# Kernel optimization log

Hardware: AMD Instinct MI355X
Metric: run time of the kernel (lower is better)

Reference implementation:

```python
import jax, jax.numpy as jnp
from jax import lax
import numpy as np

B, IMG_H, IMG_W = 8, 256, 512
NUM_CLASSES, P = 20, 32
SCALE, TOPK, IOU_THR = 32.0, 100, 0.5


def conv2d(x, w, b, stride=1, pad=1):
    y = lax.conv_general_dilated(x, w, (stride, stride), [(pad, pad), (pad, pad)],
                                 dimension_numbers=('NCHW', 'OIHW', 'NCHW'))
    return y + b[None, :, None, None]


def bilinear_resize(img, out_h, out_w):
    # img: [..., H, W]; torch F.interpolate(mode='bilinear', align_corners=False)
    H, W = img.shape[-2], img.shape[-1]
    def idx_w(n_in, n_out):
        src = (jnp.arange(n_out, dtype=jnp.float32) + 0.5) * (n_in / n_out) - 0.5
        src = jnp.clip(src, 0.0, n_in - 1)
        i0 = jnp.floor(src).astype(jnp.int32)
        i1 = jnp.minimum(i0 + 1, n_in - 1)
        return i0, i1, src - i0.astype(jnp.float32)
    y0, y1, wy = idx_w(H, out_h)
    x0, x1, wx = idx_w(W, out_w)
    top = img[..., y0, :] * (1.0 - wy)[:, None] + img[..., y1, :] * wy[:, None]
    return top[..., x0] * (1.0 - wx) + top[..., x1] * wx


def generate_anchors(fh, fw):
    ys = (jnp.arange(fh, dtype=jnp.float32) + 0.5) * (IMG_H / fh)
    xs = (jnp.arange(fw, dtype=jnp.float32) + 0.5) * (IMG_W / fw)
    cy, cx = jnp.meshgrid(ys, xs, indexing='ij')
    h = SCALE / 2
    return jnp.stack([cx - h, cy - h, cx + h, cy + h], -1).reshape(-1, 4)


def delta_to_boxes(anchors, deltas):
    a_c = (anchors[:, :2] + anchors[:, 2:]) / 2
    a_wh = anchors[:, 2:] - anchors[:, :2]
    pc = a_c + deltas[..., :2] * a_wh
    pwh = a_wh * jnp.exp(deltas[..., 2:])
    return jnp.concatenate([pc - pwh / 2, pc + pwh / 2], -1)


def nms_single(boxes, scores, labels):
    # torchvision batched_nms: offset boxes per label, greedy NMS, return kept idxs
    N = boxes.shape[0]
    off = labels.astype(boxes.dtype) * (jnp.max(boxes) + 1.0)
    b = boxes + off[:, None]
    order = jnp.argsort(-scores)
    bs = b[order]
    area = (bs[:, 2] - bs[:, 0]) * (bs[:, 3] - bs[:, 1])
    lt = jnp.maximum(bs[:, None, :2], bs[None, :, :2])
    rb = jnp.minimum(bs[:, None, 2:], bs[None, :, 2:])
    wh = jnp.clip(rb - lt, 0.0)
    inter = wh[..., 0] * wh[..., 1]
    iou = inter / (area[:, None] + area[None, :] - inter + 1e-9)
    idxs = jnp.arange(N)
    def body(i, suppressed):
        keep_i = jnp.logical_not(suppressed[i])
        row = (iou[i] > IOU_THR) & (idxs > i)
        return jnp.where(keep_i, suppressed | row, suppressed)
    suppressed = lax.fori_loop(0, N, body, jnp.zeros(N, bool))
    keep_mask = ~suppressed
    rank = jnp.cumsum(keep_mask) - 1
    slots = jnp.where(keep_mask & (rank < TOPK), rank, TOPK)
    out = jnp.full(TOPK + 1, -1, jnp.int32).at[slots].set(order.astype(jnp.int32))
    return out[:TOPK]


def setup_inputs():
    key = jax.random.key(0)
    ks = jax.random.split(key, 17)
    def cw(k, o, i, kh, kw_):
        return jax.random.normal(k, (o, i, kh, kw_), jnp.float32) / np.sqrt(i * kh * kw_)
    return {
        'images': jax.random.normal(ks[0], (B, 3, IMG_H, IMG_W), jnp.float32),
        'w1': cw(ks[1], 64, 3, 3, 3),   'b1': jnp.zeros(64, jnp.float32),
        'w2': cw(ks[2], 128, 64, 3, 3), 'b2': jnp.zeros(128, jnp.float32),
        'w3': cw(ks[3], 256, 128, 3, 3),'b3': jnp.zeros(256, jnp.float32),
        'pw1': cw(ks[4], 256, 256, 3, 3), 'pb1': jnp.zeros(256, jnp.float32),
        'pw2': cw(ks[5], P, 256, 1, 1),   'pb2': jnp.zeros(P, jnp.float32),
        'cw_': cw(ks[6], NUM_CLASSES + 1, 256, 3, 3), 'cb': jnp.zeros(NUM_CLASSES + 1, jnp.float32),
        'bw': cw(ks[7], 4, 256, 3, 3),  'bb': jnp.zeros(4, jnp.float32),
        'kw': cw(ks[8], P, 256, 3, 3),  'kb': jnp.zeros(P, jnp.float32),
    }


def reference(images, w1, b1, w2, b2, w3, b3, pw1, pb1, pw2, pb2, cw_, cb, bw, bb, kw, kb):
    x = jax.nn.relu(conv2d(images, w1, b1, stride=2))
    x = jax.nn.relu(conv2d(x, w2, b2, stride=2))
    feat = jax.nn.relu(conv2d(x, w3, b3, stride=2))          # [B,256,32,64]
    proto = conv2d(jax.nn.relu(conv2d(feat, pw1, pb1)), pw2, pb2, pad=0)  # [B,P,32,64]
    fh, fw = feat.shape[2], feat.shape[3]
    def head(w, b, c):
        return conv2d(feat, w, b).transpose(0, 2, 3, 1).reshape(B, -1, c)
    cls = head(cw_, cb, NUM_CLASSES + 1)     # [B,N,C+1]
    box = head(bw, bb, 4)                    # [B,N,4]
    coef = head(kw, kb, P)                   # [B,N,P]
    anchors = generate_anchors(fh, fw)       # [N,4]
    probs = jax.nn.softmax(cls, -1)[..., :-1]
    scores = probs.max(-1)
    labels = probs.argmax(-1).astype(jnp.int32)
    boxes = delta_to_boxes(anchors, box)     # [B,N,4]
    keep = jax.vmap(nms_single)(boxes, scores, labels)   # [B,100], -1 pad
    valid = keep >= 0
    ki = jnp.clip(keep, 0)
    take = lambda a: jnp.take_along_axis(a, ki[..., None] if a.ndim == 3 else ki, axis=1)
    boxes_k = take(boxes) * valid[..., None]
    scores_k = take(scores) * valid
    labels_k = jnp.where(valid, take(labels), 0)
    coef_k = jnp.take_along_axis(coef, ki[..., None], axis=1)   # [B,100,P]
    m = jax.nn.sigmoid(jnp.einsum('bkp,bphw->bkhw', coef_k, proto))
    masks = bilinear_resize(m, IMG_H, IMG_W) > 0.5
    masks = masks & valid[..., None, None]
    return boxes_k, scores_k, labels_k, masks, valid
```

## Files before the change

kernel.cpp:

```cpp
#include <hip/hip_runtime.h>
#include <hip/hip_bf16.h>
#include <math.h>

#define BB 8
#define NCLS 21
#define NANCH 2048
#define TOPK_N 100

static const size_t OFF_X1HI = 0;
static const size_t OFF_X1LO = 34344960;
static const size_t OFF_X2HI = 68689920;
static const size_t OFF_X2LO = 86261760;
static const size_t OFF_FTHI = 103833600;
static const size_t OFF_FTLO = 113025024;
static const size_t OFF_WT1  = 122216448;
static const size_t OFF_A2H  = 122223616;
static const size_t OFF_A2L  = 122371072;
static const size_t OFF_A3H  = 122518528;
static const size_t OFF_A3L  = 123108352;
static const size_t OFF_AHH  = 123698176;
static const size_t OFF_AHL  = 123993088;
static const size_t OFF_AP1H = 124288000;
static const size_t OFF_AP1L = 125467648;
static const size_t OFF_WTP2 = 126647296;
static const size_t OFF_BH   = 126680064;
static const size_t OFF_HOUT = 126680576;
static const size_t OFF_P1   = 130874880;
static const size_t OFF_PROTO= 147652096;
static const size_t OFF_BOXES= 149749248;
static const size_t OFF_SCORES=150011392;
static const size_t OFF_LABELS=150076928;
static const size_t OFF_ORDER= 150142464;
static const size_t OFF_SB   = 150208000;
static const size_t OFF_IOU  = 150470144;
static const size_t OFF_KEEP = 154664448;
static const size_t OFF_MAXB = 154668032;
static const size_t OFF_M    = 154668544;

static const size_t OUT_BOXES  = 0;
static const size_t OUT_SCORES = 3200;
static const size_t OUT_LABELS = 4000;
static const size_t OUT_MASKS  = 4800;
static const size_t OUT_VALID  = 104862400;

typedef __attribute__((ext_vector_type(8))) short bf16x8;
typedef __attribute__((ext_vector_type(4))) float f32x4;

__device__ __forceinline__ unsigned encf(float f){
  unsigned u = __float_as_uint(f);
  return (u & 0x80000000u) ? ~u : (u | 0x80000000u);
}
__device__ __forceinline__ float decf(unsigned u){
  unsigned b = (u & 0x80000000u) ? (u & 0x7fffffffu) : ~u;
  return __uint_as_float(b);
}
__device__ __forceinline__ short f2bf(float f){
  __hip_bfloat16 h = __float2bfloat16(f);
  return *(short*)&h;
}
__device__ __forceinline__ float bf2f(short h){
  return __uint_as_float(((unsigned)(unsigned short)h) << 16);
}

template<int CH8,int Hp,int Wp>
__global__ void halok(short* __restrict__ hi, short* __restrict__ lo,
                      unsigned* __restrict__ maxb){
  constexpr int PER = 2*Wp + 2*(Hp-2);
  int i = blockIdx.x*256 + threadIdx.x;
  if (maxb && i < BB) maxb[i] = 0u;
  if (i >= BB*CH8*PER) return;
  int cell = i % PER; int bg = i / PER;
  int y, x;
  if (cell < Wp)        { y = 0;      x = cell; }
  else if (cell < 2*Wp) { y = Hp-1;   x = cell - Wp; }
  else { int r = cell - 2*Wp; y = 1 + (r>>1); x = (r&1) ? (Wp-1) : 0; }
  size_t ad = (((size_t)bg*Hp + y)*Wp + x)*8;
  bf16x8 z = (bf16x8){0,0,0,0,0,0,0,0};
  *(bf16x8*)(hi + ad) = z;
  *(bf16x8*)(lo + ad) = z;
}

template<int CIN,int COUT,int KK>
__global__ void packw(const float* __restrict__ w, float* __restrict__ wT){
  int i = blockIdx.x*256 + threadIdx.x;
  if (i >= CIN*KK*COUT) return;
  int co = i % COUT; int r = i / COUT;
  int ci = r / KK,  k = r % KK;
  wT[i] = w[(co*CIN + ci)*KK + k];
}

template<int CIN,int COUT>
__global__ void packA(const float* __restrict__ w, short* __restrict__ Ahi,
                      short* __restrict__ Alo){
  constexpr int K = CIN*9;
  constexpr int KS = K/32;
  int i = blockIdx.x*256 + threadIdx.x;
  if (i >= COUT*K) return;
  int sub  = i & 7;
  int lane = (i >> 3) & 63;
  int rest = i >> 9;
  int ks = rest % KS;
  int mt = rest / KS;
  int m = mt*16 + (lane & 15);
  int k = ks*32 + (lane >> 4)*8 + sub;
  int tap = k / CIN, ci = k - tap*CIN;
  float v = w[(m*CIN + ci)*9 + tap];
  short h = f2bf(v);
  Ahi[i] = h;
  Alo[i] = f2bf(v - bf2f(h));
}

__global__ void packAh(const float* __restrict__ cw, const float* __restrict__ bw,
                       const float* __restrict__ kw, const float* __restrict__ cb,
                       const float* __restrict__ bb, const float* __restrict__ kb,
                       short* __restrict__ Ahi, short* __restrict__ Alo,
                       float* __restrict__ bh){
  int i = blockIdx.x*256 + threadIdx.x;
  if (i < 64){
    float v = 0.f;
    if (i < 21) v = cb[i]; else if (i < 25) v = bb[i-21]; else if (i < 57) v = kb[i-25];
    bh[i] = v;
  }
  if (i >= 64*2304) return;
  constexpr int KS = 72;
  int sub  = i & 7;
  int lane = (i >> 3) & 63;
  int rest = i >> 9;
  int ks = rest % KS;
  int mt = rest / KS;
  int m = mt*16 + (lane & 15);
  int k = ks*32 + (lane >> 4)*8 + sub;
  int tap = k >> 8, ci = k & 255;
  float v = 0.f;
  if (m < 21)      v = cw[(m*256 + ci)*9 + tap];
  else if (m < 25) v = bw[((m-21)*256 + ci)*9 + tap];
  else if (m < 57) v = kw[((m-25)*256 + ci)*9 + tap];
  short h = f2bf(v);
  Ahi[i] = h;
  Alo[i] = f2bf(v - bf2f(h));
}

__global__ __launch_bounds__(256) void conv1k(const float* __restrict__ img,
    const float* __restrict__ wT, const float* __restrict__ bias,
    short* __restrict__ x1hi, short* __restrict__ x1lo){
  const int b   = blockIdx.z;
  const int co0 = blockIdx.y * 16;
  const int g   = blockIdx.x*256 + threadIdx.x;
  const int y  = g >> 7;
  const int x0 = (g & 127) << 1;

  float acc[16][2];
#pragma unroll
  for (int c=0;c<16;c++){
    float bv = bias[co0+c];
    acc[c][0] = bv; acc[c][1] = bv;
  }
  int   off[3][5];
  float msk[3][5];
#pragma unroll
  for (int kh=0;kh<3;kh++){
    int iy = y*2 - 1 + kh;
    bool okr = (iy >= 0) && (iy < 256);
    int ro = okr ? iy*512 : 0;
#pragma unroll
    for (int t=0;t<5;t++){
      int col = x0*2 - 1 + t;
      bool ok = okr && (col >= 0) && (col < 512);
      off[kh][t] = ok ? (ro + col) : 0;
      msk[kh][t] = ok ? 1.f : 0.f;
    }
  }
  const float* inb = img + (size_t)b*3*256*512;
  for (int ci=0; ci<3; ci++){
    const float* inc = inb + (size_t)ci*256*512;
    float v[3][5];
#pragma unroll
    for (int kh=0;kh<3;kh++)
#pragma unroll
      for (int t=0;t<5;t++)
        v[kh][t] = inc[off[kh][t]] * msk[kh][t];
    const float* wp = wT + ci*9*64 + co0;
#pragma unroll
    for (int kh=0;kh<3;kh++)
#pragma unroll
    for (int kw=0;kw<3;kw++){
      const float* wq = wp + (kh*3+kw)*64;
#pragma unroll
      for (int c=0;c<16;c++){
        float wv = wq[c];
        acc[c][0] = fmaf(wv, v[kh][2*0+kw], acc[c][0]);
        acc[c][1] = fmaf(wv, v[kh][2*1+kw], acc[c][1]);
      }
    }
  }
#pragma unroll
  for (int s=0;s<2;s++){
    short hv[16] __attribute__((aligned(16)));
    short lv[16] __attribute__((aligned(16)));
#pragma unroll
    for (int c=0;c<16;c++){
      float r = fmaxf(acc[c][s], 0.f);
      short h = f2bf(r);
      hv[c] = h;
      lv[c] = f2bf(r - bf2f(h));
    }
#pragma unroll
    for (int g2=0; g2<2; g2++){
      size_t ad = (((size_t)(b*8 + (co0>>3) + g2)*130 + (y+1))*258 + (x0+s+1))*8;
      *(bf16x8*)(x1hi + ad) = *(bf16x8*)(hv + g2*8);
      *(bf16x8*)(x1lo + ad) = *(bf16x8*)(lv + g2*8);
    }
  }
}

template<int CIN,int K,int M,int MW,int NW,int S,int IPH,int IPW,int NXB,
         bool SPLIT,bool STAGELO,int EMODE,int OPH,int OPW>
__global__ __launch_bounds__(NW*64) void cgemm_row(
    const short* __restrict__ Ahi, const short* __restrict__ Alo,
    const short* __restrict__ Bhi, const short* __restrict__ Blo,
    const float* __restrict__ bias, float* __restrict__ outf,
    short* __restrict__ outhi, short* __restrict__ outlo){
  static_assert(CIN % 32 == 0, "CIN must be multiple of 32");
  static_assert(EMODE == 0 || NXB == 1, "flat out assumes OW=64");
  constexpr int NT = 64*32;
  constexpr int KS = K/32;
  constexpr int CG = CIN/8;
  constexpr int SW  = 64*S + 2;
  constexpr int SWP = (S==2) ? (SW/2 + 1) : SW;
  constexpr int PARS = (S==2) ? 2 : 1;
  constexpr int LOOFF = CG*PARS*SWP*8;
  constexpr int BUFS = (SPLIT && STAGELO) ? 2 : 1;
  __shared__ __align__(16) short sB[BUFS*LOOFF];

  const int b    = blockIdx.z;
  const int oy   = blockIdx.x / NXB;
  const int xb   = (blockIdx.x % NXB) * 64;
  const int wave = threadIdx.x >> 6;
  const int lane = threadIdx.x & 63;
  const int lm = lane & 15, lq = lane >> 4;
  const int m0 = (blockIdx.y * NW + wave) * (MW*16);
  const int tid = threadIdx.x;

  f32x4 acc[MW][4];
#pragma unroll
  for (int i=0;i<MW;i++)
#pragma unroll
    for (int j=0;j<4;j++) acc[i][j] = (f32x4){0.f,0.f,0.f,0.f};

  const short* Ah_l = Ahi + (size_t)lane*8;
  const short* Al_l = Alo + (size_t)lane*8;
  const int mt0 = m0 >> 4;
  const size_t plane = (size_t)IPH*IPW;
  const short* Bl0 = Blo + ((size_t)b*CG + lq)*plane*8;

#pragma unroll 1
  for (int dy=0; dy<3; dy++){
    const int iy = oy*S + dy;
    __syncthreads();
    {
      const short* srch = Bhi + (((size_t)b*CG*IPH + iy)*IPW + (size_t)(xb*S))*8;
      for (int c = tid; c < CG*SW; c += NW*64){
        int g = c / SW, p = c - g*SW;
        int dst = (S==2) ? ((g*2 + (p&1))*SWP + (p>>1)) : (g*SW + p);
        *(bf16x8*)(&sB[(size_t)dst*8]) =
          *(const bf16x8*)(srch + ((size_t)g*plane + p)*8);
      }
      if constexpr (SPLIT && STAGELO){
        const short* srcl = Blo + (((size_t)b*CG*IPH + iy)*IPW + (size_t)(xb*S))*8;
        for (int c = tid; c < CG*SW; c += NW*64){
          int g = c / SW, p = c - g*SW;
          int dst = (S==2) ? ((g*2 + (p&1))*SWP + (p>>1)) : (g*SW + p);
          *(bf16x8*)(&sB[LOOFF + (size_t)dst*8]) =
            *(const bf16x8*)(srcl + ((size_t)g*plane + p)*8);
        }
      }
    }
    __syncthreads();
#pragma unroll
    for (int dx=0; dx<3; dx++){
      const int tap = dy*3 + dx;
      const int ksb = tap*(CIN/32);
      for (int kc=0; kc<CIN; kc+=32){
        const int ks = ksb + (kc>>5);
        int ra[4];
#pragma unroll
        for (int j=0;j<4;j++){
          int pc = (j*16 + lm)*S + dx;
          ra[j] = (S==2) ? ((((kc>>3) + lq)*2 + (pc&1))*SWP + (pc>>1))
                         : (((kc>>3) + lq)*SW + pc);
        }
        bf16x8 ah[MW], bh_[4];
#pragma unroll
        for (int i=0;i<MW;i++)
          ah[i] = *(const bf16x8*)(Ah_l + ((size_t)(mt0+i)*KS + ks)*512);
#pragma unroll
        for (int j=0;j<4;j++)
          bh_[j] = *(const bf16x8*)(&sB[(size_t)ra[j]*8]);
        if constexpr (SPLIT){
          bf16x8 al[MW], bl_[4];
#pragma unroll
          for (int i=0;i<MW;i++)
            al[i] = *(const bf16x8*)(Al_l + ((size_t)(mt0+i)*KS + ks)*512);
          if constexpr (STAGELO){
#pragma unroll
            for (int j=0;j<4;j++)
              bl_[j] = *(const bf16x8*)(&sB[LOOFF + (size_t)ra[j]*8]);
          } else {
#pragma unroll
            for (int j=0;j<4;j++){
              size_t pix = (size_t)iy*IPW + (size_t)((xb + j*16 + lm)*S + dx);
              bl_[j] = *(const bf16x8*)(Bl0 + ((size_t)(kc>>3)*plane + pix)*8);
            }
          }
#pragma unroll
          for (int j=0;j<4;j++)
#pragma unroll
            for (int i=0;i<MW;i++)
              acc[i][j] = __builtin_amdgcn_mfma_f32_16x16x32_bf16(ah[i], bh_[j], acc[i][j], 0,0,0);
#pragma unroll
          for (int j=0;j<4;j++)
#pragma unroll
            for (int i=0;i<MW;i++)
              acc[i][j] = __builtin_amdgcn_mfma_f32_16x16x32_bf16(ah[i], bl_[j], acc[i][j], 0,0,0);
#pragma unroll
          for (int j=0;j<4;j++)
#pragma unroll
            for (int i=0;i<MW;i++)
              acc[i][j] = __builtin_amdgcn_mfma_f32_16x16x32_bf16(al[i], bh_[j], acc[i][j], 0,0,0);
        } else {
#pragma unroll
          for (int j=0;j<4;j++)
#pragma unroll
            for (int i=0;i<MW;i++)
              acc[i][j] = __builtin_amdgcn_mfma_f32_16x16x32_bf16(ah[i], bh_[j], acc[i][j], 0,0,0);
        }
      }
    }
  }

#pragma unroll
  for (int i=0;i<MW;i++){
#pragma unroll
    for (int r=0;r<4;r++){
      const int m = m0 + i*16 + lq*4 + r;
      const float bv = bias[m];
      if constexpr (EMODE == 0){
#pragma unroll
        for (int j=0;j<4;j++){
          const int ox = xb + j*16 + lm;
          float v = fmaxf(acc[i][j][r] + bv, 0.f);
          short h = f2bf(v);
          short l = f2bf(v - bf2f(h));
          size_t ad = ((((size_t)(b*(M/8) + (m>>3))*OPH + (oy+1))*OPW + (ox+1)))*8 + (m&7);
          outhi[ad] = h;
          outlo[ad] = l;
        }
      } else {
        float* cp = outf + ((size_t)b*M + m)*NT + oy*64 + lm;
#pragma unroll
        for (int j=0;j<4;j++){
          float v = acc[i][j][r] + bv;
          if constexpr (EMODE == 2) v = fmaxf(v, 0.f);
          cp[j*16] = v;
        }
      }
    }
  }
}

__global__ __launch_bounds__(256) void pw2k2(const float* __restrict__ p1,
    const float* __restrict__ wT, const float* __restrict__ bias,
    float* __restrict__ proto){
  const int b  = blockIdx.y;
  const int sp = blockIdx.x*256 + threadIdx.x;
  float acc[32];
#pragma unroll
  for (int c=0;c<32;c++) acc[c] = bias[c];
  const float* pb = p1 + (size_t)b*256*NANCH + sp;
  for (int ci=0;ci<256;ci++){
    float v = pb[(size_t)ci*NANCH];
    const float* wq = wT + ci*32;
#pragma unroll
    for (int c=0;c<32;c++) acc[c] = fmaf(v, wq[c], acc[c]);
  }
#pragma unroll
  for (int c=0;c<32;c++)
    proto[((size_t)b*32 + c)*NANCH + sp] = acc[c];
}

__global__ void decodek(const float* __restrict__ hout,
                        float* __restrict__ boxes, float* __restrict__ scores,
                        int* __restrict__ labels, unsigned* __restrict__ maxb){
  const int b = blockIdx.y;
  const int n = blockIdx.x*blockDim.x + threadIdx.x;
  const float* cp = hout + (size_t)b*64*NANCH + n;
  float l[NCLS];
  float M = -1e30f;
#pragma unroll
  for (int c=0;c<NCLS;c++){ l[c] = cp[(size_t)c*NANCH]; M = fmaxf(M, l[c]); }
  float denom = 0.f;
#pragma unroll
  for (int c=0;c<NCLS;c++) denom += expf(l[c]-M);
  float best = -1.f; int bi = 0;
#pragma unroll
  for (int c=0;c<NCLS-1;c++){
    float e = expf(l[c]-M);
    if (e > best){ best = e; bi = c; }
  }
  scores[(size_t)b*NANCH + n] = best/denom;
  labels[(size_t)b*NANCH + n] = bi;

  float dx = cp[21*(size_t)NANCH], dy = cp[22*(size_t)NANCH];
  float dw = cp[23*(size_t)NANCH], dh = cp[24*(size_t)NANCH];
  const int yy = n >> 6, xx = n & 63;
  float cx = (xx+0.5f)*8.f, cy = (yy+0.5f)*8.f;
  float px = cx + dx*32.f, py = cy + dy*32.f;
  float pw = 32.f*expf(dw), ph = 32.f*expf(dh);
  float x1 = px - 0.5f*pw, y1 = py - 0.5f*ph;
  float x2 = px + 0.5f*pw, y2 = py + 0.5f*ph;
  float* bo = boxes + ((size_t)b*NANCH + n)*4;
  bo[0]=x1; bo[1]=y1; bo[2]=x2; bo[3]=y2;
  float mx = fmaxf(fmaxf(x1,y1), fmaxf(x2,y2));
#pragma unroll
  for (int off=32; off>0; off>>=1) mx = fmaxf(mx, __shfl_down(mx, off));
  if ((threadIdx.x & 63) == 0) atomicMax(maxb + b, encf(mx));
}

__global__ void __launch_bounds__(1024) sortk(const float* __restrict__ scores,
                     const float* __restrict__ boxes, const int* __restrict__ labels,
                     const unsigned* __restrict__ maxb,
                     int* __restrict__ order, float* __restrict__ sb){
  __shared__ float sc[NANCH];
  __shared__ int   id[NANCH];
  const int b = blockIdx.x, t = threadIdx.x;
  for (int i=t;i<NANCH;i+=1024){ sc[i]=scores[(size_t)b*NANCH+i]; id[i]=i; }
  __syncthreads();
  for (int k=2;k<=NANCH;k<<=1){
    for (int j=k>>1;j>0;j>>=1){
      for (int i=t;i<NANCH;i+=1024){
        int ixj = i ^ j;
        if (ixj > i){
          float sa=sc[i], sb_=sc[ixj]; int ia=id[i], ib=id[ixj];
          bool dir = ((i & k) == 0);
          bool before_ba = (sb_ > sa) || (sb_ == sa && ib < ia);
          if (before_ba == dir){ sc[i]=sb_; sc[ixj]=sa; id[i]=ib; id[ixj]=ia; }
        }
      }
      __syncthreads();
    }
  }
  float mboff = decf(maxb[b]) + 1.0f;
  for (int r=t;r<NANCH;r+=1024){
    int o = id[r];
    order[(size_t)b*NANCH + r] = o;
    float off = (float)labels[(size_t)b*NANCH + o] * mboff;
    const float* bo = boxes + ((size_t)b*NANCH + o)*4;
    float* sp = sb + ((size_t)b*NANCH + r)*4;
    sp[0]=bo[0]+off; sp[1]=bo[1]+off; sp[2]=bo[2]+off; sp[3]=bo[3]+off;
  }
}

__global__ void ioumask(const float* __restrict__ sb, unsigned long long* __restrict__ iou){
  const int b = blockIdx.y;
  const int gid = blockIdx.x*blockDim.x + threadIdx.x;
  const int i = gid >> 5, w = gid & 31;
  const float* base = sb + (size_t)b*NANCH*4;
  unsigned long long bits = 0ull;
  const int j0 = w << 6;
  if (j0 + 63 > i){
    float x1=base[i*4], y1=base[i*4+1], x2=base[i*4+2], y2=base[i*4+3];
    float ai = (x2-x1)*(y2-y1);
    for (int jj=0;jj<64;jj++){
      int j = j0 + jj;
      if (j > i){
        float bx1=base[j*4], by1=base[j*4+1], bx2=base[j*4+2], by2=base[j*4+3];
        float lx=fmaxf(x1,bx1), ly=fmaxf(y1,by1);
        float rx=fminf(x2,bx2), ry=fminf(y2,by2);
        float ww=fmaxf(rx-lx,0.f), hh=fmaxf(ry-ly,0.f);
        float inter = ww*hh;
        float aj = (bx2-bx1)*(by2-by1);
        float v = inter/(ai + aj - inter + 1e-9f);
        if (v > 0.5f) bits |= (1ull << jj);
      }
    }
  }
  iou[((size_t)b*NANCH + i)*32 + w] = bits;
}

__global__ void nmsscan(const unsigned long long* __restrict__ iou,
                        const int* __restrict__ order, int* __restrict__ keep){
  const int b = blockIdx.x, lane = threadIdx.x;
  unsigned long long sup = 0ull;
  int k = 0;
  for (int i=0; i<NANCH && k<TOPK_N; i++){
    int wi = i >> 6, bi = i & 63;
    unsigned long long wv = __shfl(sup, wi);
    if (!((wv >> bi) & 1ull)){
      if (lane == 0) keep[b*TOPK_N + k] = order[(size_t)b*NANCH + i];
      k++;
      unsigned long long row = (lane < 32) ? iou[((size_t)b*NANCH + i)*32 + lane] : 0ull;
      sup |= row;
    }
  }
  for (int r = lane; r < TOPK_N; r += 64)
    if (r >= k) keep[b*TOPK_N + r] = -1;
}

__global__ void gatherk(const int* __restrict__ keep, const float* __restrict__ boxes,
                        const float* __restrict__ scores, const int* __restrict__ labels,
                        float* __restrict__ out){
  const int b = blockIdx.x, r = threadIdx.x;
  if (r >= TOPK_N) return;
  int ki = keep[b*TOPK_N + r];
  float valid = (ki >= 0) ? 1.f : 0.f;
  int kc = (ki < 0) ? 0 : ki;
  const float* bo = boxes + ((size_t)b*NANCH + kc)*4;
#pragma unroll
  for (int c=0;c<4;c++) out[OUT_BOXES + ((size_t)b*TOPK_N + r)*4 + c] = bo[c]*valid;
  out[OUT_SCORES + b*TOPK_N + r] = scores[(size_t)b*NANCH + kc]*valid;
  out[OUT_LABELS + b*TOPK_N + r] = (ki >= 0) ? (float)labels[(size_t)b*NANCH + kc] : 0.f;
  out[OUT_VALID  + b*TOPK_N + r] = valid;
}

__global__ void maskm(const int* __restrict__ keep, const float* __restrict__ hout,
                      const float* __restrict__ proto, float* __restrict__ m){
  const int b = blockIdx.z, r = blockIdx.y;
  int ki = keep[b*TOPK_N + r];
  if (ki < 0) return;
  const int s = blockIdx.x*blockDim.x + threadIdx.x;
  __shared__ float cf[32];
  if (threadIdx.x < 32)
    cf[threadIdx.x] = hout[((size_t)b*64 + 25 + threadIdx.x)*NANCH + ki];
  __syncthreads();
  float acc = 0.f;
#pragma unroll
  for (int p=0;p<32;p++) acc = fmaf(cf[p], proto[((size_t)b*32 + p)*NANCH + s], acc);
  m[((size_t)b*TOPK_N + r)*NANCH + s] = 1.f/(1.f + expf(-acc));
}

__global__ void resizek(const float* __restrict__ m, const int* __restrict__ keep,
                        float* __restrict__ out){
  const int b = blockIdx.z, r = blockIdx.y;
  const int pid = blockIdx.x*blockDim.x + threadIdx.x;
  const int y  = pid >> 7;
  const int x4 = (pid & 127) << 2;
  float* dst = out + OUT_MASKS + (((size_t)b*TOPK_N + r)*256 + y)*512 + x4;
  bool valid = keep[b*TOPK_N + r] >= 0;
  if (!valid){
    *(float4*)dst = make_float4(0.f,0.f,0.f,0.f);
    return;
  }
  const float* mb = m + ((size_t)b*TOPK_N + r)*NANCH;
  float sy = (y + 0.5f)*0.125f - 0.5f;
  sy = fminf(fmaxf(sy, 0.f), 31.f);
  int y0 = (int)floorf(sy);
  int y1 = min(y0+1, 31);
  float wy = sy - (float)y0;
  const float* r0 = mb + y0*64;
  const float* r1 = mb + y1*64;
  float res[4];
#pragma unroll
  for (int k=0;k<4;k++){
    int x = x4 + k;
    float sx = (x + 0.5f)*0.125f - 0.5f;
    sx = fminf(fmaxf(sx, 0.f), 63.f);
    int x0 = (int)floorf(sx);
    int x1 = min(x0+1, 63);
    float wx = sx - (float)x0;
    float t0 = r0[x0]*(1.f-wy) + r1[x0]*wy;
    float t1 = r0[x1]*(1.f-wy) + r1[x1]*wy;
    float v  = t0*(1.f-wx) + t1*wx;
    res[k] = (v > 0.5f) ? 1.f : 0.f;
  }
  *(float4*)dst = make_float4(res[0], res[1], res[2], res[3]);
}

extern "C" void kernel_launch(void* const* d_in, const int* in_sizes, int n_in,
                              void* d_out, int out_size, void* d_ws, size_t ws_size,
                              hipStream_t stream) {
  const float* images=(const float*)d_in[0];
  const float* w1=(const float*)d_in[1];  const float* b1=(const float*)d_in[2];
  const float* w2=(const float*)d_in[3];  const float* b2=(const float*)d_in[4];
  const float* w3=(const float*)d_in[5];  const float* b3=(const float*)d_in[6];
  const float* pw1=(const float*)d_in[7]; const float* pb1=(const float*)d_in[8];
  const float* pw2=(const float*)d_in[9]; const float* pb2=(const float*)d_in[10];
  const float* cw=(const float*)d_in[11]; const float* cb=(const float*)d_in[12];
  const float* bw=(const float*)d_in[13]; const float* bb=(const float*)d_in[14];
  const float* kw=(const float*)d_in[15]; const float* kb=(const float*)d_in[16];
  float* out = (float*)d_out;
  char* ws = (char*)d_ws;

  short* x1hi = (short*)(ws + OFF_X1HI);
  short* x1lo = (short*)(ws + OFF_X1LO);
  short* x2hi = (short*)(ws + OFF_X2HI);
  short* x2lo = (short*)(ws + OFF_X2LO);
  short* fthi = (short*)(ws + OFF_FTHI);
  short* ftlo = (short*)(ws + OFF_FTLO);
  float* wT1  = (float*)(ws + OFF_WT1);
  short* a2h  = (short*)(ws + OFF_A2H);
  short* a2l  = (short*)(ws + OFF_A2L);
  short* a3h  = (short*)(ws + OFF_A3H);
  short* a3l  = (short*)(ws + OFF_A3L);
  short* ahh  = (short*)(ws + OFF_AHH);
  short* ahl  = (short*)(ws + OFF_AHL);
  short* ap1h = (short*)(ws + OFF_AP1H);
  short* ap1l = (short*)(ws + OFF_AP1L);
  float* wTp2 = (float*)(ws + OFF_WTP2);
  float* bh   = (float*)(ws + OFF_BH);
  float* hout = (float*)(ws + OFF_HOUT);
  float* p1   = (float*)(ws + OFF_P1);
  float* proto= (float*)(ws + OFF_PROTO);
  float* boxes= (float*)(ws + OFF_BOXES);
  float* scores=(float*)(ws + OFF_SCORES);
  int*   labels=(int*)  (ws + OFF_LABELS);
  int*   order =(int*)  (ws + OFF_ORDER);
  float* sb   = (float*)(ws + OFF_SB);
  unsigned long long* iou = (unsigned long long*)(ws + OFF_IOU);
  int*   keep = (int*)  (ws + OFF_KEEP);
  unsigned* maxb = (unsigned*)(ws + OFF_MAXB);
  float* m    = (float*)(ws + OFF_M);

  halok<8,130,258><<<dim3(193), 256, 0, stream>>>(x1hi, x1lo, maxb);
  halok<16,66,130><<<dim3(194), 256, 0, stream>>>(x2hi, x2lo, nullptr);
  halok<32,34,66> <<<dim3(196), 256, 0, stream>>>(fthi, ftlo, nullptr);

  packw<3,64,9>  <<<dim3(7),    256, 0, stream>>>(w1, wT1);
  packA<64,128>  <<<dim3(288),  256, 0, stream>>>(w2, a2h, a2l);
  packA<128,256> <<<dim3(1152), 256, 0, stream>>>(w3, a3h, a3l);
  packA<256,256> <<<dim3(2304), 256, 0, stream>>>(pw1, ap1h, ap1l);
  packAh<<<dim3(576), 256, 0, stream>>>(cw, bw, kw, cb, bb, kb, ahh, ahl, bh);
  packw<256,32,1><<<dim3(32),   256, 0, stream>>>(pw2, wTp2);

  conv1k<<<dim3(64,4,BB), 256, 0, stream>>>(images, wT1, b1, x1hi, x1lo);

  cgemm_row<64,576,128,2,4,2,130,258,2,true,true,0,66,130>
      <<<dim3(128,1,BB), 256, 0, stream>>>(a2h, a2l, x1hi, x1lo, b2, nullptr, x2hi, x2lo);

  cgemm_row<128,1152,256,2,4,2,66,130,1,true,true,0,34,66>
      <<<dim3(32,2,BB), 256, 0, stream>>>(a3h, a3l, x2hi, x2lo, b3, nullptr, fthi, ftlo);

  cgemm_row<256,2304,64,1,4,1,34,66,1,true,true,1,1,1>
      <<<dim3(32,1,BB), 256, 0, stream>>>(ahh, ahl, fthi, ftlo, bh, hout, nullptr, nullptr);

  cgemm_row<256,2304,256,2,4,1,34,66,1,false,false,2,1,1>
      <<<dim3(32,2,BB), 256, 0, stream>>>(ap1h, ap1l, fthi, fthi, pb1, p1, nullptr, nullptr);

  pw2k2<<<dim3(8,BB), 256, 0, stream>>>(p1, wTp2, pb2, proto);

  decodek<<<dim3(8,BB), 256, 0, stream>>>(hout, boxes, scores, labels, maxb);
  sortk<<<dim3(BB), 1024, 0, stream>>>(scores, boxes, labels, maxb, order, sb);
  ioumask<<<dim3(256,BB), 256, 0, stream>>>(sb, iou);
  nmsscan<<<dim3(BB), 64, 0, stream>>>(iou, order, keep);
  gatherk<<<dim3(BB), 128, 0, stream>>>(keep, boxes, scores, labels, out);

  maskm<<<dim3(8,TOPK_N,BB), 256, 0, stream>>>(keep, hout, proto, m);
  resizek<<<dim3(128,TOPK_N,BB), 256, 0, stream>>>(m, keep, out);
}
```

Before: 960.6 us.

## Fuse setup, heads+pw1 GEMM, NMS+gather, and mask compute+resize kernels

New measurement: 979.4 us. About the same (+2.0%).

```diff
diff --git a/kernel.cpp b/kernel.cpp
--- a/kernel.cpp
+++ b/kernel.cpp
@@ -35,7 +35,6 @@
 static const size_t OFF_IOU  = 150470144;
 static const size_t OFF_KEEP = 154664448;
 static const size_t OFF_MAXB = 154668032;
-static const size_t OFF_M    = 154668544;
 
 static const size_t OUT_BOXES  = 0;
 static const size_t OUT_SCORES = 3200;
@@ -62,14 +61,20 @@
   return __uint_as_float(((unsigned)(unsigned short)h) << 16);
 }
 
-template<int CH8,int Hp,int Wp>
-__global__ void halok(short* __restrict__ hi, short* __restrict__ lo,
-                      unsigned* __restrict__ maxb){
-  constexpr int PER = 2*Wp + 2*(Hp-2);
+__global__ void halok3(short* __restrict__ x1hi, short* __restrict__ x1lo,
+                       short* __restrict__ x2hi, short* __restrict__ x2lo,
+                       short* __restrict__ fthi, short* __restrict__ ftlo,
+                       unsigned* __restrict__ maxb){
   int i = blockIdx.x*256 + threadIdx.x;
-  if (maxb && i < BB) maxb[i] = 0u;
-  if (i >= BB*CH8*PER) return;
-  int cell = i % PER; int bg = i / PER;
+  if (i < BB) maxb[i] = 0u;
+  short *hi, *lo; int Hp, Wp, cell, bg;
+  if (i < 49408){
+    hi=x1hi; lo=x1lo; Hp=130; Wp=258; cell = i % 772; bg = i / 772;
+  } else if (i < 99072){
+    int j = i - 49408; hi=x2hi; lo=x2lo; Hp=66; Wp=130; cell = j % 388; bg = j / 388;
+  } else if (i < 149248){
+    int j = i - 99072; hi=fthi; lo=ftlo; Hp=34; Wp=66; cell = j % 196; bg = j / 196;
+  } else return;
   int y, x;
   if (cell < Wp)        { y = 0;      x = cell; }
   else if (cell < 2*Wp) { y = Hp-1;   x = cell - Wp; }
@@ -81,8 +86,8 @@
 }
 
 template<int CIN,int COUT,int KK>
-__global__ void packw(const float* __restrict__ w, float* __restrict__ wT){
-  int i = blockIdx.x*256 + threadIdx.x;
+__device__ __forceinline__ void packw_body(int i, const float* __restrict__ w,
+                                           float* __restrict__ wT){
   if (i >= CIN*KK*COUT) return;
   int co = i % COUT; int r = i / COUT;
   int ci = r / KK,  k = r % KK;
@@ -90,11 +95,10 @@
 }
 
 template<int CIN,int COUT>
-__global__ void packA(const float* __restrict__ w, short* __restrict__ Ahi,
-                      short* __restrict__ Alo){
+__device__ __forceinline__ void packA_body(int i, const float* __restrict__ w,
+                                           short* __restrict__ Ahi, short* __restrict__ Alo){
   constexpr int K = CIN*9;
   constexpr int KS = K/32;
-  int i = blockIdx.x*256 + threadIdx.x;
   if (i >= COUT*K) return;
   int sub  = i & 7;
   int lane = (i >> 3) & 63;
@@ -110,12 +114,11 @@
   Alo[i] = f2bf(v - bf2f(h));
 }
 
-__global__ void packAh(const float* __restrict__ cw, const float* __restrict__ bw,
-                       const float* __restrict__ kw, const float* __restrict__ cb,
-                       const float* __restrict__ bb, const float* __restrict__ kb,
-                       short* __restrict__ Ahi, short* __restrict__ Alo,
-                       float* __restrict__ bh){
-  int i = blockIdx.x*256 + threadIdx.x;
+__device__ __forceinline__ void packAh_body(int i,
+    const float* __restrict__ cw, const float* __restrict__ bw,
+    const float* __restrict__ kw, const float* __restrict__ cb,
+    const float* __restrict__ bb, const float* __restrict__ kb,
+    short* __restrict__ Ahi, short* __restrict__ Alo, float* __restrict__ bh){
   if (i < 64){
     float v = 0.f;
     if (i < 21) v = cb[i]; else if (i < 25) v = bb[i-21]; else if (i < 57) v = kb[i-25];
@@ -140,6 +143,24 @@
   Alo[i] = f2bf(v - bf2f(h));
 }
 
+__global__ void packall(const float* __restrict__ w1, float* __restrict__ wT1,
+                        const float* __restrict__ w2, short* __restrict__ a2h, short* __restrict__ a2l,
+                        const float* __restrict__ w3, short* __restrict__ a3h, short* __restrict__ a3l,
+                        const float* __restrict__ pw1, short* __restrict__ ap1h, short* __restrict__ ap1l,
+                        const float* __restrict__ cw, const float* __restrict__ bw,
+                        const float* __restrict__ kw, const float* __restrict__ cb,
+                        const float* __restrict__ bb, const float* __restrict__ kb,
+                        short* __restrict__ ahh, short* __restrict__ ahl, float* __restrict__ bh,
+                        const float* __restrict__ pw2, float* __restrict__ wTp2){
+  int blk = blockIdx.x, t = threadIdx.x;
+  if (blk < 288)        packA_body<64,128>(blk*256+t, w2, a2h, a2l);
+  else if (blk < 1440)  packA_body<128,256>((blk-288)*256+t, w3, a3h, a3l);
+  else if (blk < 3744)  packA_body<256,256>((blk-1440)*256+t, pw1, ap1h, ap1l);
+  else if (blk < 4320)  packAh_body((blk-3744)*256+t, cw,bw,kw,cb,bb,kb, ahh,ahl,bh);
+  else if (blk < 4327)  packw_body<3,64,9>((blk-4320)*256+t, w1, wT1);
+  else                  packw_body<256,32,1>((blk-4327)*256+t, pw2, wTp2);
+}
+
 __global__ __launch_bounds__(256) void conv1k(const float* __restrict__ img,
     const float* __restrict__ wT, const float* __restrict__ bias,
     short* __restrict__ x1hi, short* __restrict__ x1lo){
@@ -221,7 +242,6 @@
     const float* __restrict__ bias, float* __restrict__ outf,
     short* __restrict__ outhi, short* __restrict__ outlo){
   static_assert(CIN % 32 == 0, "CIN must be multiple of 32");
-  static_assert(EMODE == 0 || NXB == 1, "flat out assumes OW=64");
   constexpr int NT = 64*32;
   constexpr int KS = K/32;
   constexpr int CG = CIN/8;
@@ -364,6 +384,114 @@
           cp[j*16] = v;
         }
       }
+    }
+  }
+}
+
+__global__ __launch_bounds__(256) void headspw1(
+    const short* __restrict__ Ahh, const short* __restrict__ Ahl,
+    const short* __restrict__ Aph,
+    const short* __restrict__ Bhi, const short* __restrict__ Blo,
+    const float* __restrict__ biash, const float* __restrict__ biasp,
+    float* __restrict__ hout, float* __restrict__ p1){
+  constexpr int KS = 72;
+  constexpr int CG = 32;
+  constexpr int SW = 66;
+  constexpr int IPH = 34, IPW = 66;
+  constexpr int LOOFF = CG*SW*8;
+  __shared__ __align__(16) short sB[2*LOOFF];
+
+  const int b = blockIdx.z;
+  const int oy = blockIdx.x;
+  const int wave = threadIdx.x >> 6;
+  const int lane = threadIdx.x & 63;
+  const int lm = lane & 15, lq = lane >> 4;
+  const int tid = threadIdx.x;
+
+  f32x4 acch[4];
+  f32x4 accp[4][4];
+#pragma unroll
+  for (int j=0;j<4;j++) acch[j] = (f32x4){0.f,0.f,0.f,0.f};
+#pragma unroll
+  for (int i=0;i<4;i++)
+#pragma unroll
+    for (int j=0;j<4;j++) accp[i][j] = (f32x4){0.f,0.f,0.f,0.f};
+
+  const short* Ah_l = Ahh + (size_t)lane*8;
+  const short* Al_l = Ahl + (size_t)lane*8;
+  const short* Ap_l = Aph + (size_t)lane*8;
+  const size_t plane = (size_t)IPH*IPW;
+
+#pragma unroll 1
+  for (int dy=0; dy<3; dy++){
+    const int iy = oy + dy;
+    __syncthreads();
+    {
+      const short* srch = Bhi + ((size_t)b*CG*IPH + iy)*IPW*8;
+      const short* srcl = Blo + ((size_t)b*CG*IPH + iy)*IPW*8;
+      for (int c = tid; c < CG*SW; c += 256){
+        int g = c / SW, p = c - g*SW;
+        *(bf16x8*)(&sB[(size_t)c*8]) =
+          *(const bf16x8*)(srch + ((size_t)g*plane + p)*8);
+        *(bf16x8*)(&sB[LOOFF + (size_t)c*8]) =
+          *(const bf16x8*)(srcl + ((size_t)g*plane + p)*8);
+      }
+    }
+    __syncthreads();
+#pragma unroll
+    for (int dx=0; dx<3; dx++){
+      const int tap = dy*3 + dx;
+      const int ksb = tap*8;
+      for (int kc=0; kc<256; kc+=32){
+        const int ks = ksb + (kc>>5);
+        int ra[4];
+#pragma unroll
+        for (int j=0;j<4;j++) ra[j] = ((kc>>3) + lq)*SW + (j*16 + lm) + dx;
+        bf16x8 bh_[4], bl_[4];
+#pragma unroll
+        for (int j=0;j<4;j++){
+          bh_[j] = *(const bf16x8*)(&sB[(size_t)ra[j]*8]);
+          bl_[j] = *(const bf16x8*)(&sB[LOOFF + (size_t)ra[j]*8]);
+        }
+        bf16x8 ah = *(const bf16x8*)(Ah_l + ((size_t)wave*KS + ks)*512);
+        bf16x8 al = *(const bf16x8*)(Al_l + ((size_t)wave*KS + ks)*512);
+#pragma unroll
+        for (int j=0;j<4;j++)
+          acch[j] = __builtin_amdgcn_mfma_f32_16x16x32_bf16(ah, bh_[j], acch[j], 0,0,0);
+#pragma unroll
+        for (int j=0;j<4;j++)
+          acch[j] = __builtin_amdgcn_mfma_f32_16x16x32_bf16(ah, bl_[j], acch[j], 0,0,0);
+#pragma unroll
+        for (int j=0;j<4;j++)
+          acch[j] = __builtin_amdgcn_mfma_f32_16x16x32_bf16(al, bh_[j], acch[j], 0,0,0);
+#pragma unroll
+        for (int i=0;i<4;i++){
+          bf16x8 ap = *(const bf16x8*)(Ap_l + ((size_t)(wave*4+i)*KS + ks)*512);
+#pragma unroll
+          for (int j=0;j<4;j++)
+            accp[i][j] = __builtin_amdgcn_mfma_f32_16x16x32_bf16(ap, bh_[j], accp[i][j], 0,0,0);
+        }
+      }
+    }
+  }
+
+#pragma unroll
+  for (int r=0;r<4;r++){
+    const int mh = wave*16 + lq*4 + r;
+    const float bv = biash[mh];
+    float* cp = hout + ((size_t)b*64 + mh)*NANCH + oy*64 + lm;
+#pragma unroll
+    for (int j=0;j<4;j++) cp[j*16] = acch[j][r] + bv;
+  }
+#pragma unroll
+  for (int i=0;i<4;i++){
+#pragma unroll
+    for (int r=0;r<4;r++){
+      const int mp = wave*64 + i*16 + lq*4 + r;
+      const float bv = biasp[mp];
+      float* cp = p1 + ((size_t)b*256 + mp)*NANCH + oy*64 + lm;
+#pragma unroll
+      for (int j=0;j<4;j++) cp[j*16] = fmaxf(accp[i][j][r] + bv, 0.f);
     }
   }
 }
@@ -487,92 +615,99 @@
   iou[((size_t)b*NANCH + i)*32 + w] = bits;
 }
 
-__global__ void nmsscan(const unsigned long long* __restrict__ iou,
-                        const int* __restrict__ order, int* __restrict__ keep){
+__global__ void nmsgather(const unsigned long long* __restrict__ iou,
+                          const int* __restrict__ order,
+                          const float* __restrict__ boxes, const float* __restrict__ scores,
+                          const int* __restrict__ labels,
+                          int* __restrict__ keep, float* __restrict__ out){
   const int b = blockIdx.x, lane = threadIdx.x;
+  __shared__ int s_keep[TOPK_N];
   unsigned long long sup = 0ull;
-  int k = 0;
-  for (int i=0; i<NANCH && k<TOPK_N; i++){
-    int wi = i >> 6, bi = i & 63;
-    unsigned long long wv = __shfl(sup, wi);
-    if (!((wv >> bi) & 1ull)){
-      if (lane == 0) keep[b*TOPK_N + k] = order[(size_t)b*NANCH + i];
-      k++;
-      unsigned long long row = (lane < 32) ? iou[((size_t)b*NANCH + i)*32 + lane] : 0ull;
-      sup |= row;
-    }
-  }
-  for (int r = lane; r < TOPK_N; r += 64)
-    if (r >= k) keep[b*TOPK_N + r] = -1;
-}
-
-__global__ void gatherk(const int* __restrict__ keep, const float* __restrict__ boxes,
-                        const float* __restrict__ scores, const int* __restrict__ labels,
-                        float* __restrict__ out){
-  const int b = blockIdx.x, r = threadIdx.x;
-  if (r >= TOPK_N) return;
+  int k = 0, i = 0;
+  while (k < TOPK_N){
+    unsigned long long avail = (lane < 32) ? ~sup : 0ull;
+    const int wi = i >> 6;
+    if (lane < wi) avail = 0ull;
+    else if (lane == wi) avail &= (~0ull) << (i & 63);
+    unsigned long long ball = __ballot(avail != 0ull);
+    if (!ball) break;
+    int w0 = (int)__builtin_ctzll(ball);
+    unsigned long long aw = __shfl(avail, w0);
+    int b0 = (int)__builtin_ctzll(aw);
+    i = (w0 << 6) + b0;
+    int ov = order[(size_t)b*NANCH + i];
+    if (lane == 0) s_keep[k] = ov;
+    k++;
+    unsigned long long row = (lane < 32) ? iou[((size_t)b*NANCH + i)*32 + lane] : 0ull;
+    sup |= row;
+    i++;
+    if (i >= NANCH) break;
+  }
+  __syncthreads();
+  for (int r = lane; r < TOPK_N; r += 64){
+    int kv = (r < k) ? s_keep[r] : -1;
+    keep[b*TOPK_N + r] = kv;
+    float valid = (kv >= 0) ? 1.f : 0.f;
+    int kc = (kv < 0) ? 0 : kv;
+    const float* bo = boxes + ((size_t)b*NANCH + kc)*4;
+#pragma unroll
+    for (int c=0;c<4;c++) out[OUT_BOXES + ((size_t)b*TOPK_N + r)*4 + c] = bo[c]*valid;
+    out[OUT_SCORES + b*TOPK_N + r] = scores[(size_t)b*NANCH + kc]*valid;
+    out[OUT_LABELS + b*TOPK_N + r] = (kv >= 0) ? (float)labels[(size_t)b*NANCH + kc] : 0.f;
+    out[OUT_VALID  + b*TOPK_N + r] = valid;
+  }
+}
+
+__global__ __launch_bounds__(256) void maskresize(const int* __restrict__ keep,
+    const float* __restrict__ hout, const float* __restrict__ proto,
+    float* __restrict__ out){
+  const int b = blockIdx.y, r = blockIdx.x;
+  float* obase = out + OUT_MASKS + ((size_t)b*TOPK_N + r)*131072;
   int ki = keep[b*TOPK_N + r];
-  float valid = (ki >= 0) ? 1.f : 0.f;
-  int kc = (ki < 0) ? 0 : ki;
-  const float* bo = boxes + ((size_t)b*NANCH + kc)*4;
-#pragma unroll
-  for (int c=0;c<4;c++) out[OUT_BOXES + ((size_t)b*TOPK_N + r)*4 + c] = bo[c]*valid;
-  out[OUT_SCORES + b*TOPK_N + r] = scores[(size_t)b*NANCH + kc]*valid;
-  out[OUT_LABELS + b*TOPK_N + r] = (ki >= 0) ? (float)labels[(size_t)b*NANCH + kc] : 0.f;
-  out[OUT_VALID  + b*TOPK_N + r] = valid;
-}
-
-__global__ void maskm(const int* __restrict__ keep, const float* __restrict__ hout,
-                      const float* __restrict__ proto, float* __restrict__ m){
-  const int b = blockIdx.z, r = blockIdx.y;
-  int ki = keep[b*TOPK_N + r];
-  if (ki < 0) return;
-  const int s = blockIdx.x*blockDim.x + threadIdx.x;
+  if (ki < 0){
+    float4 z = make_float4(0.f,0.f,0.f,0.f);
+    for (int idx = threadIdx.x; idx < 32768; idx += 256)
+      ((float4*)obase)[idx] = z;
+    return;
+  }
   __shared__ float cf[32];
+  __shared__ float sm[NANCH];
   if (threadIdx.x < 32)
     cf[threadIdx.x] = hout[((size_t)b*64 + 25 + threadIdx.x)*NANCH + ki];
   __syncthreads();
-  float acc = 0.f;
-#pragma unroll
-  for (int p=0;p<32;p++) acc = fmaf(cf[p], proto[((size_t)b*32 + p)*NANCH + s], acc);
-  m[((size_t)b*TOPK_N + r)*NANCH + s] = 1.f/(1.f + expf(-acc));
-}
-
-__global__ void resizek(const float* __restrict__ m, const int* __restrict__ keep,
-                        float* __restrict__ out){
-  const int b = blockIdx.z, r = blockIdx.y;
-  const int pid = blockIdx.x*blockDim.x + threadIdx.x;
-  const int y  = pid >> 7;
-  const int x4 = (pid & 127) << 2;
-  float* dst = out + OUT_MASKS + (((size_t)b*TOPK_N + r)*256 + y)*512 + x4;
-  bool valid = keep[b*TOPK_N + r] >= 0;
-  if (!valid){
-    *(float4*)dst = make_float4(0.f,0.f,0.f,0.f);
-    return;
-  }
-  const float* mb = m + ((size_t)b*TOPK_N + r)*NANCH;
-  float sy = (y + 0.5f)*0.125f - 0.5f;
-  sy = fminf(fmaxf(sy, 0.f), 31.f);
-  int y0 = (int)floorf(sy);
-  int y1 = min(y0+1, 31);
-  float wy = sy - (float)y0;
-  const float* r0 = mb + y0*64;
-  const float* r1 = mb + y1*64;
-  float res[4];
-#pragma unroll
-  for (int k=0;k<4;k++){
-    int x = x4 + k;
-    float sx = (x + 0.5f)*0.125f - 0.5f;
-    sx = fminf(fmaxf(sx, 0.f), 63.f);
-    int x0 = (int)floorf(sx);
-    int x1 = min(x0+1, 63);
-    float wx = sx - (float)x0;
-    float t0 = r0[x0]*(1.f-wy) + r1[x0]*wy;
-    float t1 = r0[x1]*(1.f-wy) + r1[x1]*wy;
-    float v  = t0*(1.f-wx) + t1*wx;
-    res[k] = (v > 0.5f) ? 1.f : 0.f;
-  }
-  *(float4*)dst = make_float4(res[0], res[1], res[2], res[3]);
+  for (int s = threadIdx.x; s < NANCH; s += 256){
+    float acc = 0.f;
+#pragma unroll
+    for (int p=0;p<32;p++) acc = fmaf(cf[p], proto[((size_t)b*32 + p)*NANCH + s], acc);
+    sm[s] = 1.f/(1.f + expf(-acc));
+  }
+  __syncthreads();
+  for (int pid = threadIdx.x; pid < 32768; pid += 256){
+    const int y  = pid >> 7;
+    const int x4 = (pid & 127) << 2;
+    float sy = (y + 0.5f)*0.125f - 0.5f;
+    sy = fminf(fmaxf(sy, 0.f), 31.f);
+    int y0 = (int)floorf(sy);
+    int y1 = min(y0+1, 31);
+    float wy = sy - (float)y0;
+    const float* r0 = sm + y0*64;
+    const float* r1 = sm + y1*64;
+    float res[4];
+#pragma unroll
+    for (int kk=0;kk<4;kk++){
+      int x = x4 + kk;
+      float sx = (x + 0.5f)*0.125f - 0.5f;
+      sx = fminf(fmaxf(sx, 0.f), 63.f);
+      int x0 = (int)floorf(sx);
+      int x1 = min(x0+1, 63);
+      float wx = sx - (float)x0;
+      float t0 = r0[x0]*(1.f-wy) + r1[x0]*wy;
+      float t1 = r0[x1]*(1.f-wy) + r1[x1]*wy;
+      float v  = t0*(1.f-wx) + t1*wx;
+      res[kk] = (v > 0.5f) ? 1.f : 0.f;
+    }
+    *(float4*)(obase + y*512 + x4) = make_float4(res[0], res[1], res[2], res[3]);
+  }
 }
 
 extern "C" void kernel_launch(void* const* d_in, const int* in_sizes, int n_in,
@@ -618,41 +753,30 @@
   unsigned long long* iou = (unsigned long long*)(ws + OFF_IOU);
   int*   keep = (int*)  (ws + OFF_KEEP);
   unsigned* maxb = (unsigned*)(ws + OFF_MAXB);
-  float* m    = (float*)(ws + OFF_M);
-
-  halok<8,130,258><<<dim3(193), 256, 0, stream>>>(x1hi, x1lo, maxb);
-  halok<16,66,130><<<dim3(194), 256, 0, stream>>>(x2hi, x2lo, nullptr);
-  halok<32,34,66> <<<dim3(196), 256, 0, stream>>>(fthi, ftlo, nullptr);
-
-  packw<3,64,9>  <<<dim3(7),    256, 0, stream>>>(w1, wT1);
-  packA<64,128>  <<<dim3(288),  256, 0, stream>>>(w2, a2h, a2l);
-  packA<128,256> <<<dim3(1152), 256, 0, stream>>>(w3, a3h, a3l);
-  packA<256,256> <<<dim3(2304), 256, 0, stream>>>(pw1, ap1h, ap1l);
-  packAh<<<dim3(576), 256, 0, stream>>>(cw, bw, kw, cb, bb, kb, ahh, ahl, bh);
-  packw<256,32,1><<<dim3(32),   256, 0, stream>>>(pw2, wTp2);
+
+  halok3<<<dim3(583), 256, 0, stream>>>(x1hi, x1lo, x2hi, x2lo, fthi, ftlo, maxb);
+
+  packall<<<dim3(4359), 256, 0, stream>>>(w1, wT1, w2, a2h, a2l, w3, a3h, a3l,
+                                          pw1, ap1h, ap1l, cw, bw, kw, cb, bb, kb,
+                                          ahh, ahl, bh, pw2, wTp2);
 
   conv1k<<<dim3(64,4,BB), 256, 0, stream>>>(images, wT1, b1, x1hi, x1lo);
 
   cgemm_row<64,576,128,2,4,2,130,258,2,true,true,0,66,130>
       <<<dim3(128,1,BB), 256, 0, stream>>>(a2h, a2l, x1hi, x1lo, b2, nullptr, x2hi, x2lo);
 
-  cgemm_row<128,1152,256,2,4,2,66,130,1,true,true,0,34,66>
-      <<<dim3(32,2,BB), 256, 0, stream>>>(a3h, a3l, x2hi, x2lo, b3, nullptr, fthi, ftlo);
-
-  cgemm_row<256,2304,64,1,4,1,34,66,1,true,true,1,1,1>
-      <<<dim3(32,1,BB), 256, 0, stream>>>(ahh, ahl, fthi, ftlo, bh, hout, nullptr, nullptr);
-
-  cgemm_row<256,2304,256,2,4,1,34,66,1,false,false,2,1,1>
-      <<<dim3(32,2,BB), 256, 0, stream>>>(ap1h, ap1l, fthi, fthi, pb1, p1, nullptr, nullptr);
+  cgemm_row<128,1152,256,2,8,2,66,130,1,true,true,0,34,66>
+      <<<dim3(32,1,BB), 512, 0, stream>>>(a3h, a3l, x2hi, x2lo, b3, nullptr, fthi, ftlo);
+
+  headspw1<<<dim3(32,1,BB), 256, 0, stream>>>(ahh, ahl, ap1h, fthi, ftlo,
+                                              bh, pb1, hout, p1);
 
   pw2k2<<<dim3(8,BB), 256, 0, stream>>>(p1, wTp2, pb2, proto);
 
   decodek<<<dim3(8,BB), 256, 0, stream>>>(hout, boxes, scores, labels, maxb);
   sortk<<<dim3(BB), 1024, 0, stream>>>(scores, boxes, labels, maxb, order, sb);
   ioumask<<<dim3(256,BB), 256, 0, stream>>>(sb, iou);
-  nmsscan<<<dim3(BB), 64, 0, stream>>>(iou, order, keep);
-  gatherk<<<dim3(BB), 128, 0, stream>>>(keep, boxes, scores, labels, out);
-
-  maskm<<<dim3(8,TOPK_N,BB), 256, 0, stream>>>(keep, hout, proto, m);
-  resizek<<<dim3(128,TOPK_N,BB), 256, 0, stream>>>(m, keep, out);
-}
+  nmsgather<<<dim3(BB), 64, 0, stream>>>(iou, order, boxes, scores, labels, keep, out);
+
+  maskresize<<<dim3(TOPK_N,BB), 256, 0, stream>>>(keep, hout, proto, out);
+}
```
